# Kernel tuning notes

Hardware: AMD Instinct MI355X
Metric: run time of the kernel (lower is better)

The kernel has to match this reference:

```python
import jax, jax.numpy as jnp
import numpy as np

B, L, D = 2, 2048, 2048
H, HKV, HD = 32, 8, 64
EPS = 1e-5
THETA = 1000000.0


def rms_norm(x, w):
    # normalize over last dim (head_dim)
    return x * jax.lax.rsqrt(jnp.mean(x * x, axis=-1, keepdims=True) + EPS) * w


def apply_rope(t):
    # t: (B, heads, L, HD); non-traditional (half-split) RoPE, offset=0
    half = HD // 2
    inv_freq = THETA ** (-jnp.arange(0, HD, 2, dtype=jnp.float32) / HD)  # (half,)
    ang = jnp.arange(L, dtype=jnp.float32)[:, None] * inv_freq           # (L, half)
    cos, sin = jnp.cos(ang), jnp.sin(ang)
    x1, x2 = t[..., :half], t[..., half:]
    return jnp.concatenate([x1 * cos - x2 * sin, x2 * cos + x1 * sin], axis=-1)


def setup_inputs() -> dict:
    key = jax.random.key(0)
    ks = jax.random.split(key, 5)
    s = 0.02
    return {
        "x": jax.random.normal(ks[0], (B, L, D), dtype=jnp.float32),
        "Wq": jax.random.normal(ks[1], (D, H * HD), dtype=jnp.float32) * s,
        "Wk": jax.random.normal(ks[2], (D, HKV * HD), dtype=jnp.float32) * s,
        "Wv": jax.random.normal(ks[3], (D, HKV * HD), dtype=jnp.float32) * s,
        "Wo": jax.random.normal(ks[4], (H * HD, D), dtype=jnp.float32) * s,
        "q_norm_w": jnp.ones((HD,), dtype=jnp.float32),
        "k_norm_w": jnp.ones((HD,), dtype=jnp.float32),
    }


def reference(x, Wq, Wk, Wv, Wo, q_norm_w, k_norm_w):
    scale = HD ** -0.5
    g = H // HKV  # GQA group size
    # projections
    q = (x @ Wq).reshape(B, L, H, HD)
    k = (x @ Wk).reshape(B, L, HKV, HD)
    v = (x @ Wv).reshape(B, L, HKV, HD)
    # per-head RMSNorm, then to (B, heads, L, HD)
    q = jnp.transpose(rms_norm(q, q_norm_w), (0, 2, 1, 3))
    k = jnp.transpose(rms_norm(k, k_norm_w), (0, 2, 1, 3))
    v = jnp.transpose(v, (0, 2, 1, 3))
    # RoPE
    q = apply_rope(q)
    k = apply_rope(k)
    # grouped-query attention with causal mask
    qg = q.reshape(B, HKV, g, L, HD)
    scores = jnp.einsum('bhgqd,bhkd->bhgqk', qg, k) * scale  # (B,HKV,g,L,L)
    causal = jnp.tril(jnp.ones((L, L), dtype=bool))
    scores = jnp.where(causal, scores, jnp.finfo(scores.dtype).min)
    probs = jax.nn.softmax(scores, axis=-1)
    out = jnp.einsum('bhgqk,bhkd->bhgqd', probs, v)           # (B,HKV,g,L,HD)
    out = jnp.transpose(out.reshape(B, H, L, HD), (0, 2, 1, 3)).reshape(B, L, H * HD)
    return out @ Wo
```

## Files before the change

kernel.cpp:

```cpp
#include <hip/hip_runtime.h>
#include <math.h>
#include <stdint.h>

#define B_ 2
#define L_ 2048
#define D_ 2048
#define H_ 32
#define HKV_ 8
#define HD_ 64
#define EPS_ 1e-5f

typedef _Float16 half_t;
typedef __attribute__((ext_vector_type(8))) _Float16 half8_t;
typedef __attribute__((ext_vector_type(4))) _Float16 half4_t;
typedef __attribute__((ext_vector_type(4))) float float4_t;

typedef const __attribute__((address_space(1))) uint32_t glb_u32;
typedef __attribute__((address_space(3))) uint32_t lds_u32;
#define GLOAD_LDS16(gp, lp) \
  __builtin_amdgcn_global_load_lds((glb_u32*)(gp), (lds_u32*)(lp), 16, 0, 0)

__device__ __forceinline__ float4_t fmax4(float4_t a, float4_t b) {
  float4_t r;
  r[0] = fmaxf(a[0], b[0]); r[1] = fmaxf(a[1], b[1]);
  r[2] = fmaxf(a[2], b[2]); r[3] = fmaxf(a[3], b[3]);
  return r;
}

__device__ __forceinline__ uint32_t pk_f16(float a, float b) {
  auto p = __builtin_amdgcn_cvt_pkrtz(a, b);
  return __builtin_bit_cast(uint32_t, p);
}

__global__ __launch_bounds__(256) void prep_all(
    const float* __restrict__ x,
    const float* __restrict__ Wq, const float* __restrict__ Wk,
    const float* __restrict__ Wv, const float* __restrict__ Wo,
    half_t* __restrict__ xh,
    half_t* __restrict__ Wqt, half_t* __restrict__ Wkt,
    half_t* __restrict__ Wvt, half_t* __restrict__ Wot)
{
  __shared__ float tile[64][65];
  const int t = threadIdx.x;
  int id = blockIdx.x;

  if (id < 4096) {
    size_t i = ((size_t)id * 256 + t) * 8;
    float4 v0 = *(const float4*)&x[i];
    float4 v1 = *(const float4*)&x[i + 4];
    half8_t h;
    h[0] = (half_t)v0.x; h[1] = (half_t)v0.y; h[2] = (half_t)v0.z; h[3] = (half_t)v0.w;
    h[4] = (half_t)v1.x; h[5] = (half_t)v1.y; h[6] = (half_t)v1.z; h[7] = (half_t)v1.w;
    *(half8_t*)&xh[i] = h;
    return;
  }
  id -= 4096;
  const float* W; half_t* Wt; int N;
  if (id < 1024)      { W = Wq; Wt = Wqt; N = 2048; }
  else if (id < 1280) { id -= 1024; W = Wk; Wt = Wkt; N = 512; }
  else if (id < 1536) { id -= 1280; W = Wv; Wt = Wvt; N = 512; }
  else                { id -= 1536; W = Wo; Wt = Wot; N = 2048; }
  const int K = 2048;
  int tk = id & 31, tn = id >> 5;
  int k0 = tk * 64, n0 = tn * 64;

  int rr = t >> 6, cc = t & 63;
#pragma unroll
  for (int i = 0; i < 16; i++)
    tile[rr + i * 4][cc] = W[(size_t)(k0 + rr + i * 4) * N + n0 + cc];
  __syncthreads();

  int rn = t >> 2, q4 = (t & 3) * 16;
  half8_t h0, h1;
#pragma unroll
  for (int u = 0; u < 8; u++) h0[u] = (half_t)tile[q4 + u][rn];
#pragma unroll
  for (int u = 0; u < 8; u++) h1[u] = (half_t)tile[q4 + 8 + u][rn];
  *(half8_t*)&Wt[(size_t)(n0 + rn) * K + k0 + q4]     = h0;
  *(half8_t*)&Wt[(size_t)(n0 + rn) * K + k0 + q4 + 8] = h1;
}

template <typename CT>
__device__ __forceinline__ void gemm_tile_f16(
    const half_t* __restrict__ A, const half_t* __restrict__ Bt,
    CT* __restrict__ C, int K, int ldc, int row0, int col0,
    bool tv, half_t* __restrict__ vtp)
{
  __shared__ __align__(16) half_t As[128 * 32];
  __shared__ __align__(16) half_t Bs[128 * 32];
  const int t    = threadIdx.x;
  const int lane = t & 63;
  const int w    = t >> 6;
  const int quad = lane >> 4, c = lane & 15;
  const int wm = (w >> 1) * 64, wn = (w & 1) * 64;

  float4_t acc[4][4];
#pragma unroll
  for (int i = 0; i < 4; i++)
#pragma unroll
    for (int j = 0; j < 4; j++) acc[i][j] = (float4_t){0.f, 0.f, 0.f, 0.f};

  const int srow = w * 32 + (lane >> 2);
  const int scol = (lane & 3) * 8;
  const half_t* Ag0 = A  + (size_t)(row0 + srow) * K + scol;
  const half_t* Ag1 = Ag0 + (size_t)16 * K;
  const half_t* Bg0 = Bt + (size_t)(col0 + srow) * K + scol;
  const half_t* Bg1 = Bg0 + (size_t)16 * K;
  half_t* As_w0 = &As[(w * 32) * 32];
  half_t* As_w1 = &As[(w * 32 + 16) * 32];
  half_t* Bs_w0 = &Bs[(w * 32) * 32];
  half_t* Bs_w1 = &Bs[(w * 32 + 16) * 32];

  for (int k0 = 0; k0 < K; k0 += 32) {
    __syncthreads();
    GLOAD_LDS16(Ag0 + k0, As_w0);
    GLOAD_LDS16(Ag1 + k0, As_w1);
    GLOAD_LDS16(Bg0 + k0, Bs_w0);
    GLOAD_LDS16(Bg1 + k0, Bs_w1);
    __syncthreads();

    half8_t af[4], bf[4];
#pragma unroll
    for (int i = 0; i < 4; i++)
      af[i] = *(const half8_t*)&As[(wm + i * 16 + c) * 32 + quad * 8];
#pragma unroll
    for (int j = 0; j < 4; j++)
      bf[j] = *(const half8_t*)&Bs[(wn + j * 16 + c) * 32 + quad * 8];
#pragma unroll
    for (int i = 0; i < 4; i++)
#pragma unroll
      for (int j = 0; j < 4; j++)
        acc[i][j] = __builtin_amdgcn_mfma_f32_16x16x32_f16(af[i], bf[j], acc[i][j], 0, 0, 0);
  }

  if (tv) {
    const int kvq = (col0 + wn) >> 6;
#pragma unroll
    for (int i = 0; i < 4; i++) {
      int row = row0 + wm + i * 16 + quad * 4;
      int bb  = row >> 11;
      int tok = row & (L_ - 1);
      half_t* vbase = vtp + (((size_t)bb * HKV_ + kvq) * HD_ + c) * L_ + tok;
#pragma unroll
      for (int j = 0; j < 4; j++) {
        half4_t h4;
#pragma unroll
        for (int r = 0; r < 4; r++) h4[r] = (half_t)acc[i][j][r];
        *(half4_t*)(vbase + (size_t)(j * 16) * L_) = h4;
      }
    }
  } else {
#pragma unroll
    for (int i = 0; i < 4; i++)
#pragma unroll
      for (int r = 0; r < 4; r++) {
        CT* Cp = C + (size_t)(row0 + wm + i * 16 + quad * 4 + r) * ldc + col0 + wn + c;
#pragma unroll
        for (int j = 0; j < 4; j++)
          Cp[j * 16] = (CT)acc[i][j][r];
      }
  }
}

__global__ __launch_bounds__(256) void qkv_gemm_h(
    const half_t* __restrict__ xh,
    const half_t* __restrict__ Wqt, const half_t* __restrict__ Wkt,
    const half_t* __restrict__ Wvt,
    half_t* __restrict__ qh, half_t* __restrict__ kh, half_t* __restrict__ vt)
{
  int lin = (int)blockIdx.y * 24 + (int)blockIdx.x;
  int xcd = lin & 7, idx = lin >> 3;
  int cy = xcd >> 2, cx = xcd & 3;
  int by = cy * 16 + idx / 6;
  int bx = cx * 6 + idx % 6;

  const half_t* Bt; half_t* C; int ldc, col0; bool tv = false;
  if (bx < 16)      { Bt = Wqt; C = qh; ldc = H_ * HD_;   col0 = bx * 128; }
  else if (bx < 20) { Bt = Wkt; C = kh; ldc = HKV_ * HD_; col0 = (bx - 16) * 128; }
  else              { Bt = Wvt; C = vt; ldc = HKV_ * HD_; col0 = (bx - 20) * 128;
                      tv = true; }
  gemm_tile_f16<half_t>(xh, Bt, C, D_, ldc, by * 128, col0, tv, vt);
}

__global__ __launch_bounds__(256) void out_gemm_h(
    const half_t* __restrict__ attn, const half_t* __restrict__ Wot,
    float* __restrict__ out)
{
  int lin = (int)blockIdx.y * 16 + (int)blockIdx.x;
  int xcd = lin & 7, idx = lin >> 3;
  int cy = xcd >> 1, cx = xcd & 1;
  int by = cy * 8 + idx / 8;
  int bx = cx * 8 + idx % 8;
  gemm_tile_f16<float>(attn, Wot, out, H_ * HD_, D_, by * 128, bx * 128,
                       false, nullptr);
}

__device__ __forceinline__ void norm_rope_row(
    half_t* __restrict__ buf, float wv, int row, int nheads, int lognh,
    int lane, float oscale, float cv, float sv)
{
  int head  = row & (nheads - 1);
  int token = row >> lognh;

  size_t idx = (size_t)token * (nheads * HD_) + head * HD_ + lane;
  float x = (float)buf[idx];

  float ss = x * x;
#pragma unroll
  for (int off = 32; off; off >>= 1) ss += __shfl_xor(ss, off);
  float xn = x * rsqrtf(ss * (1.0f / HD_) + EPS_) * wv;

  float partner = __shfl_xor(xn, 32);
  float res = (lane < 32) ? (xn * cv - partner * sv) : (xn * cv + partner * sv);
  buf[idx] = (half_t)(res * oscale);
}

__global__ __launch_bounds__(256) void postproc(
    half_t* __restrict__ qh, half_t* __restrict__ kh,
    const float* __restrict__ qw, const float* __restrict__ kw)
{
  const int t    = threadIdx.x;
  const int lane = t & 63;
  const int wv   = t >> 6;
  int id = blockIdx.x;

  int fi = lane & 31;
  float inv_freq = exp2f((float)fi * -0.622862853f);

  if (id < 8192) {
    int row0  = (id * 4 + wv) * 4;
    int token = row0 >> 5;
    int l     = token & (L_ - 1);
    float ang = (float)l * inv_freq;
    float cvv = cosf(ang), svv = sinf(ang);
    float wq  = qw[lane];
#pragma unroll
    for (int u = 0; u < 4; u++)
      norm_rope_row(qh, wq, row0 + u, H_, 5, lane, 0.180336880f, cvv, svv);
    return;
  }
  id -= 8192;
  {
    int row0  = (id * 4 + wv) * 4;
    int token = row0 >> 3;
    int l     = token & (L_ - 1);
    float ang = (float)l * inv_freq;
    float cvv = cosf(ang), svv = sinf(ang);
    float wk  = kw[lane];
#pragma unroll
    for (int u = 0; u < 4; u++)
      norm_rope_row(kh, wk, row0 + u, HKV_, 3, lane, 1.0f, cvv, svv);
  }
}

__global__ __launch_bounds__(512) void flash_mfma2(
    const half_t* __restrict__ Qh, const half_t* __restrict__ Kh,
    const half_t* __restrict__ Vt, half_t* __restrict__ Oa)
{
  __shared__ __align__(16) half_t Ks[64][72];
  __shared__ __align__(16) half_t Vs[64][72];
  __shared__ __align__(16) half_t Ps[128][72];
  __shared__ __align__(16) float  Ab[128];

  const int t    = threadIdx.x;
  const int w    = t >> 6;
  const int lane = t & 63;
  const int quad = lane >> 4;
  const int c    = lane & 15;
  const int h = blockIdx.y, b = blockIdx.z;
  const int kvh = h >> 2;

  const half_t* kbase = Kh + (size_t)(b * L_) * (HKV_ * HD_) + kvh * HD_;
  const half_t* vbase = Vt + (size_t)((b * HKV_ + kvh) * HD_) * L_;
  const int sr = t >> 3;
  const int su = (t & 7) * 8;

  half8_t ones;
#pragma unroll
  for (int u = 0; u < 8; u++) ones[u] = (half_t)1.0f;

  for (int pass = 0; pass < 2; pass++) {
    const int qb  = pass ? (15 - (int)blockIdx.x) : (int)blockIdx.x;
    const int q0  = qb * 128;
    const int wq0 = q0 + w * 16;

    half8_t qf0, qf1;
    {
      const half_t* qp = Qh + ((size_t)(b * L_ + wq0 + c)) * (H_ * HD_) + h * HD_;
      qf0 = *(const half8_t*)&qp[quad * 8];
      qf1 = *(const half8_t*)&qp[32 + quad * 8];
    }

    float4_t o[5];
#pragma unroll
    for (int dt = 0; dt < 5; dt++) o[dt] = (float4_t){0.f, 0.f, 0.f, 0.f};
    float mm = -__builtin_inff();

    half8_t kr, vr;
    kr = *(const half8_t*)(kbase + (size_t)sr * (HKV_ * HD_) + su);
    vr = *(const half8_t*)(vbase + (size_t)sr * L_ + su);

    const int last = (q0 + 127) >> 6;
    for (int kt = 0; kt <= last; kt++) {
      const int kk0 = kt * 64;
      __syncthreads();
      *(half8_t*)&Ks[sr][su] = kr;
      *(half8_t*)&Vs[sr][su] = vr;
      __syncthreads();
      if (kt < last) {
        kr = *(const half8_t*)(kbase + (size_t)(kk0 + 64 + sr) * (HKV_ * HD_) + su);
        vr = *(const half8_t*)(vbase + (size_t)sr * L_ + kk0 + 64 + su);
      }
      if (kk0 > wq0 + 15) continue;

      float4_t S[4];
      __builtin_amdgcn_s_setprio(1);
#pragma unroll
      for (int tt = 0; tt < 4; tt++) {
        half8_t kf0 = *(const half8_t*)&Ks[tt * 16 + c][quad * 8];
        half8_t kf1 = *(const half8_t*)&Ks[tt * 16 + c][32 + quad * 8];
        float4_t s = (float4_t){0.f, 0.f, 0.f, 0.f};
        s = __builtin_amdgcn_mfma_f32_16x16x32_f16(kf0, qf0, s, 0, 0, 0);
        s = __builtin_amdgcn_mfma_f32_16x16x32_f16(kf1, qf1, s, 0, 0, 0);
        S[tt] = s;
      }
      __builtin_amdgcn_s_setprio(0);

      if (kk0 + 63 > wq0) {
#pragma unroll
        for (int tt = 0; tt < 4; tt++) {
          int base = kk0 + tt * 16 + quad * 4 - (wq0 + c);
#pragma unroll
          for (int r = 0; r < 4; r++)
            if (base + r > 0) S[tt][r] = -__builtin_inff();
        }
      }

      {
        float4_t m4 = fmax4(fmax4(S[0], S[1]), fmax4(S[2], S[3]));
        float mloc = fmaxf(fmaxf(m4[0], m4[1]), fmaxf(m4[2], m4[3]));
        mloc = fmaxf(mloc, __shfl_xor(mloc, 16));
        mloc = fmaxf(mloc, __shfl_xor(mloc, 32));
        if (__any(mloc > mm + 8.0f)) {
          float mnew = fmaxf(mm, mloc);
          float al = exp2f(mm - mnew);
          mm = mnew;
          if (quad == 0) Ab[w * 16 + c] = al;
          float4_t av = *(const float4_t*)&Ab[w * 16 + quad * 4];
#pragma unroll
          for (int dt = 0; dt < 5; dt++)
#pragma unroll
            for (int r = 0; r < 4; r++) o[dt][r] *= av[r];
        }
#pragma unroll
        for (int tt = 0; tt < 4; tt++) {
#pragma unroll
          for (int r = 0; r < 4; r++) S[tt][r] = exp2f(S[tt][r] - mm);
          uint2 pw;
          pw.x = pk_f16(S[tt][0], S[tt][1]);
          pw.y = pk_f16(S[tt][2], S[tt][3]);
          *(uint2*)&Ps[w * 16 + c][tt * 16 + quad * 4] = pw;
        }
      }

      half8_t pf0 = *(const half8_t*)&Ps[w * 16 + c][quad * 8];
      half8_t pf1 = *(const half8_t*)&Ps[w * 16 + c][32 + quad * 8];
      __builtin_amdgcn_s_setprio(1);
      o[4] = __builtin_amdgcn_mfma_f32_16x16x32_f16(pf0, ones, o[4], 0, 0, 0);
      o[4] = __builtin_amdgcn_mfma_f32_16x16x32_f16(pf1, ones, o[4], 0, 0, 0);
#pragma unroll
      for (int dt = 0; dt < 4; dt++) {
        half8_t vf0 = *(const half8_t*)&Vs[dt * 16 + c][quad * 8];
        half8_t vf1 = *(const half8_t*)&Vs[dt * 16 + c][32 + quad * 8];
        o[dt] = __builtin_amdgcn_mfma_f32_16x16x32_f16(pf0, vf0, o[dt], 0, 0, 0);
        o[dt] = __builtin_amdgcn_mfma_f32_16x16x32_f16(pf1, vf1, o[dt], 0, 0, 0);
      }
      __builtin_amdgcn_s_setprio(0);
    }

#pragma unroll
    for (int r = 0; r < 4; r++) {
      float inv = 1.0f / o[4][r];
      half_t* op = Oa + ((size_t)(b * L_ + wq0 + quad * 4 + r)) * (H_ * HD_)
                 + h * HD_ + c;
#pragma unroll
      for (int dt = 0; dt < 4; dt++)
        op[dt * 16] = (half_t)(o[dt][r] * inv);
    }
  }
}

extern "C" void kernel_launch(void* const* d_in, const int* in_sizes, int n_in,
                              void* d_out, int out_size, void* d_ws, size_t ws_size,
                              hipStream_t stream)
{
  const float* x  = (const float*)d_in[0];
  const float* Wq = (const float*)d_in[1];
  const float* Wk = (const float*)d_in[2];
  const float* Wv = (const float*)d_in[3];
  const float* Wo = (const float*)d_in[4];
  const float* qw = (const float*)d_in[5];
  const float* kw = (const float*)d_in[6];
  float* out = (float*)d_out;

  const size_t XN = (size_t)B_ * L_ * D_;
  const size_t QN = (size_t)B_ * L_ * H_ * HD_;
  const size_t KN = (size_t)B_ * L_ * HKV_ * HD_;
  const size_t WQ = (size_t)D_ * H_ * HD_;
  const size_t WK = (size_t)D_ * HKV_ * HD_;

  half_t* p   = (half_t*)d_ws;
  half_t* xh  = p;  p += XN;
  half_t* Wqt = p;  p += WQ;
  half_t* Wkt = p;  p += WK;
  half_t* Wvt = p;  p += WK;
  half_t* Wot = p;  p += WQ;
  half_t* qh  = p;  p += QN;
  half_t* kh  = p;  p += KN;
  half_t* vt  = p;  p += KN;
  half_t* attn = xh;

  prep_all<<<6656, 256, 0, stream>>>(x, Wq, Wk, Wv, Wo, xh, Wqt, Wkt, Wvt, Wot);

  qkv_gemm_h<<<dim3(24, 32), 256, 0, stream>>>(xh, Wqt, Wkt, Wvt, qh, kh, vt);

  postproc<<<8192 + 2048, 256, 0, stream>>>(qh, kh, qw, kw);

  flash_mfma2<<<dim3(8, H_, B_), 512, 0, stream>>>(qh, kh, vt, attn);

  out_gemm_h<<<dim3(16, 32), 256, 0, stream>>>(attn, Wot, out);
}
```

Baseline: 315.8 us.

## Fuse Q RMSNorm and RoPE into flash attention Q-fragment load

Moves the per-head RMSNorm, RoPE and softmax-scale of Q out of the separate postproc pass and into the flash attention kernel, applied directly to the Q fragments as they are loaded. A small precomputed cos/sin table is built in the mid kernel, reusing the no-longer-needed Wqt buffer as scratch, while K normalization stays in a standalone pass. This removes a full read-modify-write pass over the Q tensor. In exchange, the attention kernel does extra per-fragment work and table loads, repeated across both passes.

Measured after the change: 316.8 us. Within noise of the previous version (+0.3%).

```diff
diff --git a/kernel.cpp b/kernel.cpp
--- a/kernel.cpp
+++ b/kernel.cpp
@@ -215,47 +215,43 @@
   buf[idx] = (half_t)(res * oscale);
 }
 
-__global__ __launch_bounds__(256) void postproc(
-    half_t* __restrict__ qh, half_t* __restrict__ kh,
-    const float* __restrict__ qw, const float* __restrict__ kw)
-{
-  const int t    = threadIdx.x;
+__global__ __launch_bounds__(256) void mid(
+    half_t* __restrict__ kh, const float* __restrict__ kw,
+    float* __restrict__ ct, float* __restrict__ st)
+{
+  const int t = threadIdx.x;
+  int id = blockIdx.x;
+
+  if (id < 256) {
+    int e = id * 256 + t;
+    int l = e >> 5, fi = e & 31;
+    float inv_freq = exp2f((float)fi * -0.622862853f);
+    float ang = (float)l * inv_freq;
+    ct[e] = cosf(ang);
+    st[e] = sinf(ang);
+    return;
+  }
+  id -= 256;
   const int lane = t & 63;
   const int wv   = t >> 6;
-  int id = blockIdx.x;
-
   int fi = lane & 31;
   float inv_freq = exp2f((float)fi * -0.622862853f);
-
-  if (id < 8192) {
-    int row0  = (id * 4 + wv) * 4;
-    int token = row0 >> 5;
-    int l     = token & (L_ - 1);
-    float ang = (float)l * inv_freq;
-    float cvv = cosf(ang), svv = sinf(ang);
-    float wq  = qw[lane];
-#pragma unroll
-    for (int u = 0; u < 4; u++)
-      norm_rope_row(qh, wq, row0 + u, H_, 5, lane, 0.180336880f, cvv, svv);
-    return;
-  }
-  id -= 8192;
-  {
-    int row0  = (id * 4 + wv) * 4;
-    int token = row0 >> 3;
-    int l     = token & (L_ - 1);
-    float ang = (float)l * inv_freq;
-    float cvv = cosf(ang), svv = sinf(ang);
-    float wk  = kw[lane];
-#pragma unroll
-    for (int u = 0; u < 4; u++)
-      norm_rope_row(kh, wk, row0 + u, HKV_, 3, lane, 1.0f, cvv, svv);
-  }
+  int row0  = (id * 4 + wv) * 4;
+  int token = row0 >> 3;
+  int l     = token & (L_ - 1);
+  float ang = (float)l * inv_freq;
+  float cvv = cosf(ang), svv = sinf(ang);
+  float wk  = kw[lane];
+#pragma unroll
+  for (int u = 0; u < 4; u++)
+    norm_rope_row(kh, wk, row0 + u, HKV_, 3, lane, 1.0f, cvv, svv);
 }
 
 __global__ __launch_bounds__(512) void flash_mfma2(
     const half_t* __restrict__ Qh, const half_t* __restrict__ Kh,
-    const half_t* __restrict__ Vt, half_t* __restrict__ Oa)
+    const half_t* __restrict__ Vt, half_t* __restrict__ Oa,
+    const float* __restrict__ qw,
+    const float* __restrict__ ct, const float* __restrict__ st)
 {
   __shared__ __align__(16) half_t Ks[64][72];
   __shared__ __align__(16) half_t Vs[64][72];
@@ -287,8 +283,38 @@
     half8_t qf0, qf1;
     {
       const half_t* qp = Qh + ((size_t)(b * L_ + wq0 + c)) * (H_ * HD_) + h * HD_;
-      qf0 = *(const half8_t*)&qp[quad * 8];
-      qf1 = *(const half8_t*)&qp[32 + quad * 8];
+      half8_t r0 = *(const half8_t*)&qp[quad * 8];
+      half8_t r1 = *(const half8_t*)&qp[32 + quad * 8];
+      float x1[8], x2[8];
+      float ss = 0.f;
+#pragma unroll
+      for (int j = 0; j < 8; j++) {
+        x1[j] = (float)r0[j]; x2[j] = (float)r1[j];
+        ss += x1[j] * x1[j] + x2[j] * x2[j];
+      }
+      ss += __shfl_xor(ss, 16);
+      ss += __shfl_xor(ss, 32);
+      float rn = rsqrtf(ss * (1.0f / HD_) + EPS_);
+      const int l = wq0 + c;
+      float4 c0 = *(const float4*)&ct[l * 32 + quad * 8];
+      float4 c1 = *(const float4*)&ct[l * 32 + quad * 8 + 4];
+      float4 s0 = *(const float4*)&st[l * 32 + quad * 8];
+      float4 s1 = *(const float4*)&st[l * 32 + quad * 8 + 4];
+      float4 w0 = *(const float4*)&qw[quad * 8];
+      float4 w1 = *(const float4*)&qw[quad * 8 + 4];
+      float4 w2 = *(const float4*)&qw[32 + quad * 8];
+      float4 w3 = *(const float4*)&qw[32 + quad * 8 + 4];
+      const float cs[8] = {c0.x, c0.y, c0.z, c0.w, c1.x, c1.y, c1.z, c1.w};
+      const float sn[8] = {s0.x, s0.y, s0.z, s0.w, s1.x, s1.y, s1.z, s1.w};
+      const float wa[8] = {w0.x, w0.y, w0.z, w0.w, w1.x, w1.y, w1.z, w1.w};
+      const float wb[8] = {w2.x, w2.y, w2.z, w2.w, w3.x, w3.y, w3.z, w3.w};
+#pragma unroll
+      for (int j = 0; j < 8; j++) {
+        float xa = x1[j] * rn * wa[j];
+        float xb = x2[j] * rn * wb[j];
+        qf0[j] = (half_t)((xa * cs[j] - xb * sn[j]) * 0.180336880f);
+        qf1[j] = (half_t)((xb * cs[j] + xa * sn[j]) * 0.180336880f);
+      }
     }
 
     float4_t o[5];
@@ -420,13 +446,16 @@
   half_t* vt  = p;  p += KN;
   half_t* attn = xh;
 
+  float* ct = (float*)Wqt;
+  float* st = ct + 65536;
+
   prep_all<<<6656, 256, 0, stream>>>(x, Wq, Wk, Wv, Wo, xh, Wqt, Wkt, Wvt, Wot);
 
   qkv_gemm_h<<<dim3(24, 32), 256, 0, stream>>>(xh, Wqt, Wkt, Wvt, qh, kh, vt);
 
-  postproc<<<8192 + 2048, 256, 0, stream>>>(qh, kh, qw, kw);
-
-  flash_mfma2<<<dim3(8, H_, B_), 512, 0, stream>>>(qh, kh, vt, attn);
+  mid<<<256 + 2048, 256, 0, stream>>>(kh, kw, ct, st);
+
+  flash_mfma2<<<dim3(8, H_, B_), 512, 0, stream>>>(qh, kh, vt, attn, qw, ct, st);
 
   out_gemm_h<<<dim3(16, 32), 256, 0, stream>>>(attn, Wot, out);
 }
```
